# Performance work log

Hardware: AMD Instinct MI355X
Metric: run time of the kernel (lower is better)

## Reference

```python
import jax, jax.numpy as jnp
import numpy as np

B, T, C = 64, 256, 384
H, HD = 6, 64


def setup_inputs() -> dict:
    key = jax.random.key(0)
    ks = jax.random.split(key, 6)
    x = jax.random.normal(ks[0], (B, T, C), dtype=jnp.float32)
    s = 1.0 / np.sqrt(C)
    Wq = jax.random.normal(ks[1], (H, C, HD), dtype=jnp.float32) * s
    Wk = jax.random.normal(ks[2], (H, C, HD), dtype=jnp.float32) * s
    Wv = jax.random.normal(ks[3], (H, C, HD), dtype=jnp.float32) * s
    Wp = jax.random.normal(ks[4], (C, C), dtype=jnp.float32) * s
    bp = jnp.zeros((C,), dtype=jnp.float32)
    return {"x": x, "Wq": Wq, "Wk": Wk, "Wv": Wv, "Wp": Wp, "bp": bp}


def reference(x, Wq, Wk, Wv, Wp, bp):
    # per-head projections (no bias), vectorized over heads
    q = jnp.einsum('btc,hcd->bhtd', x, Wq)
    k = jnp.einsum('btc,hcd->bhtd', x, Wk)
    v = jnp.einsum('btc,hcd->bhtd', x, Wv)
    scale = HD ** (-0.5)
    scores = jnp.einsum('bhtd,bhsd->bhts', q, k) * scale  # [B,H,T,T]
    causal = jnp.tril(jnp.ones((T, T), dtype=bool))
    scores = jnp.where(causal, scores, -jnp.inf)
    wei = jax.nn.softmax(scores, axis=-1)  # dropout is identity in eval mode
    out = jnp.einsum('bhts,bhsd->bhtd', wei, v)
    out = out.transpose(0, 2, 1, 3).reshape(B, T, C)  # concat heads
    return out @ Wp.T + bp
```

## Files before the change

### kernel.cpp

```cpp
#include <hip/hip_runtime.h>
#include <hip/hip_bf16.h>
#include <cstdint>
#include <cstddef>

#define B_ 64
#define T_ 256
#define C_ 384
#define H_ 6
#define HD_ 64

using u16 = unsigned short;
typedef __attribute__((ext_vector_type(8))) short short8;
typedef __attribute__((ext_vector_type(4))) short short4_;
typedef __attribute__((ext_vector_type(4))) float f32x4;

__device__ __forceinline__ u16 f2bf(float f) {
    union { float f; uint32_t u; } x{f};
    uint32_t r = x.u + 0x7fffu + ((x.u >> 16) & 1u);
    return (u16)(r >> 16);
}

__global__ void k_prep(const float* __restrict__ x, const float* __restrict__ Wq,
                       const float* __restrict__ Wk, const float* __restrict__ Wv,
                       const float* __restrict__ Wp, u16* __restrict__ xb,
                       u16* __restrict__ wqkv, u16* __restrict__ wpb) {
    int bid = blockIdx.x;
    if (bid < 3072) {
        int i = (bid * 256 + threadIdx.x) * 8;
        const f32x4* p = (const f32x4*)(x + i);
        f32x4 a = p[0], b = p[1];
        short8 s;
        s[0] = (short)f2bf(a[0]); s[1] = (short)f2bf(a[1]);
        s[2] = (short)f2bf(a[2]); s[3] = (short)f2bf(a[3]);
        s[4] = (short)f2bf(b[0]); s[5] = (short)f2bf(b[1]);
        s[6] = (short)f2bf(b[2]); s[7] = (short)f2bf(b[3]);
        *(short8*)(xb + i) = s;
    } else if (bid < 3180) {
        __shared__ u16 Tt[64 * 65];
        int pb = bid - 3072;
        int which = pb / 36, rem = pb % 36;
        int h = rem / 6, cc0 = (rem % 6) * 64;
        const float* W = (which == 0) ? Wq : ((which == 1) ? Wk : Wv);
        int d = threadIdx.x & 63, cr0 = threadIdx.x >> 6;
#pragma unroll
        for (int p = 0; p < 16; ++p) {
            int cr = p * 4 + cr0;
            Tt[cr * 65 + d] = f2bf(W[(h * 384 + cc0 + cr) * 64 + d]);
        }
        __syncthreads();
        int ccl = threadIdx.x & 63, dl0 = threadIdx.x >> 6;
        int nbase = which * 384 + h * 64;
#pragma unroll
        for (int p = 0; p < 16; ++p) {
            int dl = p * 4 + dl0;
            wqkv[(size_t)(nbase + dl) * 384 + cc0 + ccl] = Tt[ccl * 65 + dl];
        }
    } else {
        int i = ((bid - 3180) * 256 + threadIdx.x) * 8;
        const f32x4* p = (const f32x4*)(Wp + i);
        f32x4 a = p[0], b = p[1];
        short8 s;
        s[0] = (short)f2bf(a[0]); s[1] = (short)f2bf(a[1]);
        s[2] = (short)f2bf(a[2]); s[3] = (short)f2bf(a[3]);
        s[4] = (short)f2bf(b[0]); s[5] = (short)f2bf(b[1]);
        s[6] = (short)f2bf(b[2]); s[7] = (short)f2bf(b[3]);
        *(short8*)(wpb + i) = s;
    }
}

__device__ __forceinline__ void stage_tile(const u16* __restrict__ gbase, int ld,
                                           u16* lds_tile, int wid, int lane, int k0) {
#pragma unroll
    for (int i = 0; i < 4; ++i) {
        int chunk = wid * 4 + i;
        int row = chunk * 8 + (lane >> 3);
        int pslot = lane & 7;
        const u16* gp = gbase + (size_t)row * ld + k0 + ((pslot ^ (row & 7)) << 3);
        u16* lp = lds_tile + chunk * 512;
        __builtin_amdgcn_global_load_lds((const __attribute__((address_space(1))) void*)gp,
                                         (__attribute__((address_space(3))) void*)lp, 16, 0, 0);
    }
}

__device__ __forceinline__ short8 read_frag(const u16* lds_tile, int row, int ks, int g) {
    int pslot = (ks * 4 + g) ^ (row & 7);
    return *(const short8*)&lds_tile[row * 64 + pslot * 8];
}

__global__ __launch_bounds__(256, 2) void k_gemm_qkv(const u16* __restrict__ xb, const u16* __restrict__ wb,
                                                     u16* __restrict__ q, u16* __restrict__ k,
                                                     u16* __restrict__ v) {
    __shared__ alignas(16) u16 lds[2][16384];
    const int tid = threadIdx.x, lane = tid & 63, wid = tid >> 6;
    const int wm = wid >> 1, wn = wid & 1, g = lane >> 4, c = lane & 15;
    const int n0 = blockIdx.x * 128, m0 = blockIdx.y * 128;
    const u16* Ag = xb + (size_t)m0 * 384;
    const u16* Bg = wb + (size_t)n0 * 384;
    f32x4 acc[4][4] = {};
    stage_tile(Ag, 384, &lds[0][0], wid, lane, 0);
    stage_tile(Bg, 384, &lds[0][8192], wid, lane, 0);
    __syncthreads();
    int cur = 0;
    for (int t = 0; t < 6; ++t) {
        if (t < 5) {
            stage_tile(Ag, 384, &lds[cur ^ 1][0], wid, lane, (t + 1) * 64);
            stage_tile(Bg, 384, &lds[cur ^ 1][8192], wid, lane, (t + 1) * 64);
        }
        const u16* A = &lds[cur][0];
        const u16* Bm = &lds[cur][8192];
        short8 af[2][4], bf[2][4];
#pragma unroll
        for (int ks = 0; ks < 2; ++ks) {
#pragma unroll
            for (int mf = 0; mf < 4; ++mf) af[ks][mf] = read_frag(A, wm * 64 + mf * 16 + c, ks, g);
#pragma unroll
            for (int nf = 0; nf < 4; ++nf) bf[ks][nf] = read_frag(Bm, wn * 64 + nf * 16 + c, ks, g);
        }
#pragma unroll
        for (int ks = 0; ks < 2; ++ks)
#pragma unroll
            for (int mf = 0; mf < 4; ++mf)
#pragma unroll
                for (int nf = 0; nf < 4; ++nf)
                    acc[mf][nf] = __builtin_amdgcn_mfma_f32_16x16x32_bf16(af[ks][mf], bf[ks][nf], acc[mf][nf], 0, 0, 0);
        __syncthreads();
        cur ^= 1;
    }
    const int which = n0 / 384;
    u16* dst = (which == 0) ? q : ((which == 1) ? k : v);
    const int h = ((n0 + wn * 64) % 384) / 64;
#pragma unroll
    for (int mf = 0; mf < 4; ++mf)
#pragma unroll
        for (int nf = 0; nf < 4; ++nf)
#pragma unroll
            for (int r = 0; r < 4; ++r) {
                int m = m0 + wm * 64 + mf * 16 + g * 4 + r;
                int d = nf * 16 + c;
                int b = m >> 8, t = m & 255;
                dst[((b * H_ + h) * T_ + t) * HD_ + d] = f2bf(acc[mf][nf][r]);
            }
}

__global__ __launch_bounds__(256, 2) void k_attn(const u16* __restrict__ q, const u16* __restrict__ k,
                                                 const u16* __restrict__ v, u16* __restrict__ ao) {
    __shared__ u16 Kt[64 * 72];
    __shared__ u16 Vt[64 * 72];
    const int tid = threadIdx.x, bh = blockIdx.x;
    const int lane = tid & 63, wid = tid >> 6;
    const int g = lane >> 4, c = lane & 15;
    const int bq = bh * 256;

    short8 qB[4][2];
#pragma unroll
    for (int qf = 0; qf < 4; ++qf)
#pragma unroll
        for (int ks = 0; ks < 2; ++ks) {
            int t = wid * 64 + qf * 16 + c;
            qB[qf][ks] = *(const short8*)&q[(bq + t) * 64 + ks * 32 + g * 8];
        }
    float mrun[4], lrun[4];
#pragma unroll
    for (int i = 0; i < 4; ++i) { mrun[i] = -1e30f; lrun[i] = 0.f; }
    f32x4 o[4][4] = {};

    for (int kt = 0; kt < 4; ++kt) {
#pragma unroll
        for (int i = 0; i < 2; ++i) {
            int idx = tid + i * 256;
            int row = idx >> 3, c8 = (idx & 7) * 8;
            *(short8*)&Kt[row * 72 + c8] = *(const short8*)&k[(bq + kt * 64 + row) * 64 + c8];
            int vrow = idx & 63, vc8 = (idx >> 6) * 8;
            int kv = ((vrow >> 5) << 5) | (((vrow >> 2) & 3) << 3) | (((vrow >> 4) & 1) << 2) | (vrow & 3);
            short8 vv = *(const short8*)&v[(bq + kt * 64 + vrow) * 64 + vc8];
#pragma unroll
            for (int j = 0; j < 8; ++j)
                Vt[(vc8 + j) * 72 + kv] = (u16)vv[j];
        }
        __syncthreads();
        if (kt <= wid) {
            f32x4 st[4][4] = {};
#pragma unroll
            for (int ks = 0; ks < 2; ++ks) {
                short8 kA[4];
#pragma unroll
                for (int sf = 0; sf < 4; ++sf)
                    kA[sf] = *(short8*)&Kt[(sf * 16 + c) * 72 + ks * 32 + g * 8];
#pragma unroll
                for (int sf = 0; sf < 4; ++sf)
#pragma unroll
                    for (int qf = 0; qf < 4; ++qf)
                        st[sf][qf] = __builtin_amdgcn_mfma_f32_16x16x32_bf16(kA[sf], qB[qf][ks], st[sf][qf], 0, 0, 0);
            }
            float pm[4] = {-1e30f, -1e30f, -1e30f, -1e30f};
#pragma unroll
            for (int sf = 0; sf < 4; ++sf)
#pragma unroll
                for (int qf = 0; qf < 4; ++qf)
#pragma unroll
                    for (int r = 0; r < 4; ++r) {
                        float val = st[sf][qf][r] * 0.125f;
                        if (kt == wid) {
                            int s_loc = sf * 16 + g * 4 + r, q_loc = qf * 16 + c;
                            if (s_loc > q_loc) val = -1e30f;
                        }
                        st[sf][qf][r] = val;
                        pm[qf] = fmaxf(pm[qf], val);
                    }
            float alpha[4];
#pragma unroll
            for (int qf = 0; qf < 4; ++qf) {
                pm[qf] = fmaxf(pm[qf], __shfl_xor(pm[qf], 16));
                pm[qf] = fmaxf(pm[qf], __shfl_xor(pm[qf], 32));
                float mnew = fmaxf(mrun[qf], pm[qf]);
                alpha[qf] = __expf(mrun[qf] - mnew);
                mrun[qf] = mnew;
            }
            short8 pA[4][2];
#pragma unroll
            for (int qf = 0; qf < 4; ++qf) {
                float ls = 0.f;
#pragma unroll
                for (int ks = 0; ks < 2; ++ks) {
                    short8 pa;
#pragma unroll
                    for (int half = 0; half < 2; ++half) {
                        f32x4 sv = st[2 * ks + half][qf];
#pragma unroll
                        for (int r = 0; r < 4; ++r) {
                            float p = __expf(sv[r] - mrun[qf]);
                            ls += p;
                            pa[half * 4 + r] = (short)f2bf(p);
                        }
                    }
                    pA[qf][ks] = pa;
                }
                ls += __shfl_xor(ls, 16);
                ls += __shfl_xor(ls, 32);
                lrun[qf] = lrun[qf] * alpha[qf] + ls;
            }
#pragma unroll
            for (int mf = 0; mf < 4; ++mf)
#pragma unroll
                for (int r = 0; r < 4; ++r) {
                    float aof = __shfl(alpha[mf], g * 4 + r);
#pragma unroll
                    for (int df = 0; df < 4; ++df)
                        o[mf][df][r] *= aof;
                }
#pragma unroll
            for (int ks = 0; ks < 2; ++ks) {
                short8 vB[4];
#pragma unroll
                for (int df = 0; df < 4; ++df)
                    vB[df] = *(short8*)&Vt[(df * 16 + c) * 72 + ks * 32 + g * 8];
#pragma unroll
                for (int mf = 0; mf < 4; ++mf)
#pragma unroll
                    for (int df = 0; df < 4; ++df)
                        o[mf][df] = __builtin_amdgcn_mfma_f32_16x16x32_bf16(pA[mf][ks], vB[df], o[mf][df], 0, 0, 0);
            }
        }
        __syncthreads();
    }
    const int bb = bh / H_, hh = bh % H_;
#pragma unroll
    for (int mf = 0; mf < 4; ++mf)
#pragma unroll
        for (int r = 0; r < 4; ++r) {
            float inv = 1.0f / __shfl(lrun[mf], g * 4 + r);
            int t = wid * 64 + mf * 16 + g * 4 + r;
#pragma unroll
            for (int df = 0; df < 4; ++df) {
                int d = df * 16 + c;
                ao[((size_t)(bb * T_ + t)) * C_ + hh * 64 + d] = f2bf(o[mf][df][r] * inv);
            }
        }
}

__global__ __launch_bounds__(256, 2) void k_gemm_proj(const u16* __restrict__ ab, const u16* __restrict__ wp,
                                                      const float* __restrict__ bp, float* __restrict__ out) {
    __shared__ alignas(16) u16 lds[2][16384];
    const int tid = threadIdx.x, lane = tid & 63, wid = tid >> 6;
    const int wm = wid >> 1, wn = wid & 1, g = lane >> 4, c = lane & 15;
    const int n0 = blockIdx.x * 128, m0 = blockIdx.y * 128;
    const u16* Ag = ab + (size_t)m0 * 384;
    const u16* Bg = wp + (size_t)n0 * 384;
    f32x4 acc[4][4] = {};
    stage_tile(Ag, 384, &lds[0][0], wid, lane, 0);
    stage_tile(Bg, 384, &lds[0][8192], wid, lane, 0);
    __syncthreads();
    int cur = 0;
    for (int t = 0; t < 6; ++t) {
        if (t < 5) {
            stage_tile(Ag, 384, &lds[cur ^ 1][0], wid, lane, (t + 1) * 64);
            stage_tile(Bg, 384, &lds[cur ^ 1][8192], wid, lane, (t + 1) * 64);
        }
        const u16* A = &lds[cur][0];
        const u16* Bm = &lds[cur][8192];
        short8 af[2][4], bf[2][4];
#pragma unroll
        for (int ks = 0; ks < 2; ++ks) {
#pragma unroll
            for (int mf = 0; mf < 4; ++mf) af[ks][mf] = read_frag(A, wm * 64 + mf * 16 + c, ks, g);
#pragma unroll
            for (int nf = 0; nf < 4; ++nf) bf[ks][nf] = read_frag(Bm, wn * 64 + nf * 16 + c, ks, g);
        }
#pragma unroll
        for (int ks = 0; ks < 2; ++ks)
#pragma unroll
            for (int mf = 0; mf < 4; ++mf)
#pragma unroll
                for (int nf = 0; nf < 4; ++nf)
                    acc[mf][nf] = __builtin_amdgcn_mfma_f32_16x16x32_bf16(af[ks][mf], bf[ks][nf], acc[mf][nf], 0, 0, 0);
        __syncthreads();
        cur ^= 1;
    }
#pragma unroll
    for (int mf = 0; mf < 4; ++mf)
#pragma unroll
        for (int nf = 0; nf < 4; ++nf)
#pragma unroll
            for (int r = 0; r < 4; ++r) {
                int m = m0 + wm * 64 + mf * 16 + g * 4 + r;
                int n = n0 + wn * 64 + nf * 16 + c;
                out[(size_t)m * C_ + n] = acc[mf][nf][r] + bp[n];
            }
}


extern "C" void kernel_launch(void* const* d_in, const int* in_sizes, int n_in,
                              void* d_out, int out_size, void* d_ws, size_t ws_size,
                              hipStream_t stream) {
    const float* x  = (const float*)d_in[0];
    const float* Wq = (const float*)d_in[1];
    const float* Wk = (const float*)d_in[2];
    const float* Wv = (const float*)d_in[3];
    const float* Wp = (const float*)d_in[4];
    const float* bp = (const float*)d_in[5];
    float* out = (float*)d_out;

    char* ws = (char*)d_ws;
    u16* xb   = (u16*)(ws);
    u16* wqkv = (u16*)(ws + 12582912);
    u16* wpb  = (u16*)(ws + 13467648);
    u16* qb   = (u16*)(ws + 13762560);
    u16* kb   = (u16*)(ws + 26345472);
    u16* vb   = (u16*)(ws + 38928384);
    u16* ab   = (u16*)(ws + 51511296);

    k_prep<<<3252, 256, 0, stream>>>(x, Wq, Wk, Wv, Wp, xb, wqkv, wpb);
    k_gemm_qkv<<<dim3(9, 128), 256, 0, stream>>>(xb, wqkv, qb, kb, vb);
    k_attn<<<384, 256, 0, stream>>>(qb, kb, vb, ab);
    k_gemm_proj<<<dim3(3, 128), 256, 0, stream>>>(ab, wpb, bp, out);
}
```

Before: 74.12 us.

## Fuse QKV projection into the attention kernel, keeping Q/K/V on-chip

Replaces the separate QKV GEMM and attention kernels with a single kernel per (batch, head). Each block computes its head's Q, K and V from the x slice and keeps Q in registers and K/V in LDS. Attention then runs without the Q/K/V global round trip or the extra launch. The cost is that each block re-reads the full x slice for its batch (six heads share it), uses much more LDS at occupancy 1, and has only 384 blocks to spread across the GPU.

```diff
diff --git a/kernel.cpp b/kernel.cpp
--- a/kernel.cpp
+++ b/kernel.cpp
@@ -68,11 +68,12 @@
     }
 }
 
-__device__ __forceinline__ void stage_tile(const u16* __restrict__ gbase, int ld,
+template<int NROWS>
+__device__ __forceinline__ void stage_rows(const u16* __restrict__ gbase, int ld,
                                            u16* lds_tile, int wid, int lane, int k0) {
 #pragma unroll
-    for (int i = 0; i < 4; ++i) {
-        int chunk = wid * 4 + i;
+    for (int i = 0; i < NROWS / 32; ++i) {
+        int chunk = wid * (NROWS / 32) + i;
         int row = chunk * 8 + (lane >> 3);
         int pslot = lane & 7;
         const u16* gp = gbase + (size_t)row * ld + k0 + ((pslot ^ (row & 7)) << 3);
@@ -87,183 +88,193 @@
     return *(const short8*)&lds_tile[row * 64 + pslot * 8];
 }
 
-__global__ __launch_bounds__(256, 2) void k_gemm_qkv(const u16* __restrict__ xb, const u16* __restrict__ wb,
-                                                     u16* __restrict__ q, u16* __restrict__ k,
-                                                     u16* __restrict__ v) {
-    __shared__ alignas(16) u16 lds[2][16384];
+__global__ __launch_bounds__(256, 1) void k_qkv_attn(const u16* __restrict__ xb,
+                                                     const u16* __restrict__ wqkv,
+                                                     u16* __restrict__ ao) {
+    __shared__ alignas(16) u16 Kl[256 * 64];
+    __shared__ alignas(16) u16 Vt[4][64][72];
+    __shared__ alignas(16) u16 xs[256 * 64];
+    __shared__ alignas(16) u16 wsW[2][3][4096];
     const int tid = threadIdx.x, lane = tid & 63, wid = tid >> 6;
-    const int wm = wid >> 1, wn = wid & 1, g = lane >> 4, c = lane & 15;
-    const int n0 = blockIdx.x * 128, m0 = blockIdx.y * 128;
-    const u16* Ag = xb + (size_t)m0 * 384;
-    const u16* Bg = wb + (size_t)n0 * 384;
-    f32x4 acc[4][4] = {};
-    stage_tile(Ag, 384, &lds[0][0], wid, lane, 0);
-    stage_tile(Bg, 384, &lds[0][8192], wid, lane, 0);
+    const int g = lane >> 4, c = lane & 15;
+    const int bh = blockIdx.x, b = bh / H_, h = bh % H_;
+    const u16* xg = xb + (size_t)b * 256 * 384;
+    const u16* wg0 = wqkv + (size_t)(h * 64) * 384;
+    const u16* wg1 = wqkv + (size_t)(384 + h * 64) * 384;
+    const u16* wg2 = wqkv + (size_t)(768 + h * 64) * 384;
+
+    f32x4 aq[4][4] = {}, ak[4][4] = {}, av[4][4] = {};
+
+    stage_rows<256>(xg, 384, xs, wid, lane, 0);
+    stage_rows<64>(wg0, 384, &wsW[0][0][0], wid, lane, 0);
+    stage_rows<64>(wg1, 384, &wsW[0][1][0], wid, lane, 0);
+    stage_rows<64>(wg2, 384, &wsW[0][2][0], wid, lane, 0);
+    asm volatile("s_waitcnt vmcnt(0)" ::: "memory");
+    __builtin_amdgcn_sched_barrier(0);
+    __builtin_amdgcn_s_barrier();
+
+    for (int cc = 0; cc < 6; ++cc) {
+        short8 bx[2][4];
+#pragma unroll
+        for (int ks = 0; ks < 2; ++ks)
+#pragma unroll
+            for (int tf = 0; tf < 4; ++tf)
+                bx[ks][tf] = read_frag(xs, wid * 64 + tf * 16 + c, ks, g);
+        asm volatile("s_waitcnt lgkmcnt(0)" ::: "memory");
+        __builtin_amdgcn_sched_barrier(0);
+        __builtin_amdgcn_s_barrier();
+        if (cc < 5) {
+            stage_rows<256>(xg, 384, xs, wid, lane, (cc + 1) * 64);
+            stage_rows<64>(wg0, 384, &wsW[(cc + 1) & 1][0][0], wid, lane, (cc + 1) * 64);
+            stage_rows<64>(wg1, 384, &wsW[(cc + 1) & 1][1][0], wid, lane, (cc + 1) * 64);
+            stage_rows<64>(wg2, 384, &wsW[(cc + 1) & 1][2][0], wid, lane, (cc + 1) * 64);
+        }
+        const u16* Wql = &wsW[cc & 1][0][0];
+        const u16* Wkl = &wsW[cc & 1][1][0];
+        const u16* Wvl = &wsW[cc & 1][2][0];
+#pragma unroll
+        for (int ks = 0; ks < 2; ++ks) {
+            short8 fq[4], fk[4], fv[4];
+#pragma unroll
+            for (int df = 0; df < 4; ++df) {
+                fq[df] = read_frag(Wql, df * 16 + c, ks, g);
+                fk[df] = read_frag(Wkl, df * 16 + c, ks, g);
+                fv[df] = read_frag(Wvl, df * 16 + c, ks, g);
+            }
+#pragma unroll
+            for (int df = 0; df < 4; ++df)
+#pragma unroll
+                for (int tf = 0; tf < 4; ++tf) {
+                    aq[df][tf] = __builtin_amdgcn_mfma_f32_16x16x32_bf16(fq[df], bx[ks][tf], aq[df][tf], 0, 0, 0);
+                    ak[df][tf] = __builtin_amdgcn_mfma_f32_16x16x32_bf16(fk[df], bx[ks][tf], ak[df][tf], 0, 0, 0);
+                    av[tf][df] = __builtin_amdgcn_mfma_f32_16x16x32_bf16(bx[ks][tf], fv[df], av[tf][df], 0, 0, 0);
+                }
+        }
+        if (cc < 5) asm volatile("s_waitcnt vmcnt(0)" ::: "memory");
+        __builtin_amdgcn_sched_barrier(0);
+        __builtin_amdgcn_s_barrier();
+    }
+
+    short8 qB[4][2];
+#pragma unroll
+    for (int qf = 0; qf < 4; ++qf)
+#pragma unroll
+        for (int ks = 0; ks < 2; ++ks)
+#pragma unroll
+            for (int j = 0; j < 8; ++j)
+                qB[qf][ks][j] = (short)f2bf(aq[2 * ks + (j >> 2)][qf][j & 3]);
+
+#pragma unroll
+    for (int sf = 0; sf < 4; ++sf)
+#pragma unroll
+        for (int df = 0; df < 4; ++df) {
+            int row = wid * 64 + sf * 16 + c;
+            int pslot = (4 * (df >> 1) + g) ^ (row & 7);
+            short4_ k4;
+#pragma unroll
+            for (int r = 0; r < 4; ++r) k4[r] = (short)f2bf(ak[df][sf][r]);
+            *(short4_*)&Kl[row * 64 + pslot * 8 + 4 * (df & 1)] = k4;
+        }
+#pragma unroll
+    for (int sf = 0; sf < 4; ++sf)
+#pragma unroll
+        for (int df = 0; df < 4; ++df) {
+            int colb = 32 * (sf >> 1) + 8 * g + 4 * (sf & 1);
+            short4_ v4;
+#pragma unroll
+            for (int r = 0; r < 4; ++r) v4[r] = (short)f2bf(av[sf][df][r]);
+            *(short4_*)&Vt[wid][df * 16 + c][colb] = v4;
+        }
     __syncthreads();
-    int cur = 0;
-    for (int t = 0; t < 6; ++t) {
-        if (t < 5) {
-            stage_tile(Ag, 384, &lds[cur ^ 1][0], wid, lane, (t + 1) * 64);
-            stage_tile(Bg, 384, &lds[cur ^ 1][8192], wid, lane, (t + 1) * 64);
-        }
-        const u16* A = &lds[cur][0];
-        const u16* Bm = &lds[cur][8192];
-        short8 af[2][4], bf[2][4];
-#pragma unroll
-        for (int ks = 0; ks < 2; ++ks) {
-#pragma unroll
-            for (int mf = 0; mf < 4; ++mf) af[ks][mf] = read_frag(A, wm * 64 + mf * 16 + c, ks, g);
-#pragma unroll
-            for (int nf = 0; nf < 4; ++nf) bf[ks][nf] = read_frag(Bm, wn * 64 + nf * 16 + c, ks, g);
-        }
-#pragma unroll
-        for (int ks = 0; ks < 2; ++ks)
-#pragma unroll
-            for (int mf = 0; mf < 4; ++mf)
-#pragma unroll
-                for (int nf = 0; nf < 4; ++nf)
-                    acc[mf][nf] = __builtin_amdgcn_mfma_f32_16x16x32_bf16(af[ks][mf], bf[ks][nf], acc[mf][nf], 0, 0, 0);
-        __syncthreads();
-        cur ^= 1;
-    }
-    const int which = n0 / 384;
-    u16* dst = (which == 0) ? q : ((which == 1) ? k : v);
-    const int h = ((n0 + wn * 64) % 384) / 64;
-#pragma unroll
-    for (int mf = 0; mf < 4; ++mf)
-#pragma unroll
-        for (int nf = 0; nf < 4; ++nf)
-#pragma unroll
-            for (int r = 0; r < 4; ++r) {
-                int m = m0 + wm * 64 + mf * 16 + g * 4 + r;
-                int d = nf * 16 + c;
-                int b = m >> 8, t = m & 255;
-                dst[((b * H_ + h) * T_ + t) * HD_ + d] = f2bf(acc[mf][nf][r]);
-            }
-}
-
-__global__ __launch_bounds__(256, 2) void k_attn(const u16* __restrict__ q, const u16* __restrict__ k,
-                                                 const u16* __restrict__ v, u16* __restrict__ ao) {
-    __shared__ u16 Kt[64 * 72];
-    __shared__ u16 Vt[64 * 72];
-    const int tid = threadIdx.x, bh = blockIdx.x;
-    const int lane = tid & 63, wid = tid >> 6;
-    const int g = lane >> 4, c = lane & 15;
-    const int bq = bh * 256;
-
-    short8 qB[4][2];
-#pragma unroll
-    for (int qf = 0; qf < 4; ++qf)
-#pragma unroll
-        for (int ks = 0; ks < 2; ++ks) {
-            int t = wid * 64 + qf * 16 + c;
-            qB[qf][ks] = *(const short8*)&q[(bq + t) * 64 + ks * 32 + g * 8];
-        }
+
     float mrun[4], lrun[4];
 #pragma unroll
     for (int i = 0; i < 4; ++i) { mrun[i] = -1e30f; lrun[i] = 0.f; }
     f32x4 o[4][4] = {};
 
-    for (int kt = 0; kt < 4; ++kt) {
-#pragma unroll
-        for (int i = 0; i < 2; ++i) {
-            int idx = tid + i * 256;
-            int row = idx >> 3, c8 = (idx & 7) * 8;
-            *(short8*)&Kt[row * 72 + c8] = *(const short8*)&k[(bq + kt * 64 + row) * 64 + c8];
-            int vrow = idx & 63, vc8 = (idx >> 6) * 8;
-            int kv = ((vrow >> 5) << 5) | (((vrow >> 2) & 3) << 3) | (((vrow >> 4) & 1) << 2) | (vrow & 3);
-            short8 vv = *(const short8*)&v[(bq + kt * 64 + vrow) * 64 + vc8];
-#pragma unroll
-            for (int j = 0; j < 8; ++j)
-                Vt[(vc8 + j) * 72 + kv] = (u16)vv[j];
-        }
-        __syncthreads();
-        if (kt <= wid) {
-            f32x4 st[4][4] = {};
+    for (int kt = 0; kt <= wid; ++kt) {
+        f32x4 st[4][4] = {};
+#pragma unroll
+        for (int ks = 0; ks < 2; ++ks) {
+            short8 kA[4];
+#pragma unroll
+            for (int sf = 0; sf < 4; ++sf)
+                kA[sf] = read_frag(Kl, kt * 64 + sf * 16 + c, ks, g);
+#pragma unroll
+            for (int sf = 0; sf < 4; ++sf)
+#pragma unroll
+                for (int qf = 0; qf < 4; ++qf)
+                    st[sf][qf] = __builtin_amdgcn_mfma_f32_16x16x32_bf16(kA[sf], qB[qf][ks], st[sf][qf], 0, 0, 0);
+        }
+        float pm[4] = {-1e30f, -1e30f, -1e30f, -1e30f};
+#pragma unroll
+        for (int sf = 0; sf < 4; ++sf)
+#pragma unroll
+            for (int qf = 0; qf < 4; ++qf)
+#pragma unroll
+                for (int r = 0; r < 4; ++r) {
+                    float val = st[sf][qf][r] * 0.125f;
+                    if (kt == wid) {
+                        int s_loc = sf * 16 + g * 4 + r, q_loc = qf * 16 + c;
+                        if (s_loc > q_loc) val = -1e30f;
+                    }
+                    st[sf][qf][r] = val;
+                    pm[qf] = fmaxf(pm[qf], val);
+                }
+        float alpha[4];
+#pragma unroll
+        for (int qf = 0; qf < 4; ++qf) {
+            pm[qf] = fmaxf(pm[qf], __shfl_xor(pm[qf], 16));
+            pm[qf] = fmaxf(pm[qf], __shfl_xor(pm[qf], 32));
+            float mnew = fmaxf(mrun[qf], pm[qf]);
+            alpha[qf] = __expf(mrun[qf] - mnew);
+            mrun[qf] = mnew;
+        }
+        short8 pA[4][2];
+#pragma unroll
+        for (int qf = 0; qf < 4; ++qf) {
+            float ls = 0.f;
 #pragma unroll
             for (int ks = 0; ks < 2; ++ks) {
-                short8 kA[4];
-#pragma unroll
-                for (int sf = 0; sf < 4; ++sf)
-                    kA[sf] = *(short8*)&Kt[(sf * 16 + c) * 72 + ks * 32 + g * 8];
-#pragma unroll
-                for (int sf = 0; sf < 4; ++sf)
-#pragma unroll
-                    for (int qf = 0; qf < 4; ++qf)
-                        st[sf][qf] = __builtin_amdgcn_mfma_f32_16x16x32_bf16(kA[sf], qB[qf][ks], st[sf][qf], 0, 0, 0);
-            }
-            float pm[4] = {-1e30f, -1e30f, -1e30f, -1e30f};
-#pragma unroll
-            for (int sf = 0; sf < 4; ++sf)
-#pragma unroll
-                for (int qf = 0; qf < 4; ++qf)
+                short8 pa;
+#pragma unroll
+                for (int half = 0; half < 2; ++half) {
+                    f32x4 sv = st[2 * ks + half][qf];
 #pragma unroll
                     for (int r = 0; r < 4; ++r) {
-                        float val = st[sf][qf][r] * 0.125f;
-                        if (kt == wid) {
-                            int s_loc = sf * 16 + g * 4 + r, q_loc = qf * 16 + c;
-                            if (s_loc > q_loc) val = -1e30f;
-                        }
-                        st[sf][qf][r] = val;
-                        pm[qf] = fmaxf(pm[qf], val);
+                        float p = __expf(sv[r] - mrun[qf]);
+                        ls += p;
+                        pa[half * 4 + r] = (short)f2bf(p);
                     }
-            float alpha[4];
-#pragma unroll
-            for (int qf = 0; qf < 4; ++qf) {
-                pm[qf] = fmaxf(pm[qf], __shfl_xor(pm[qf], 16));
-                pm[qf] = fmaxf(pm[qf], __shfl_xor(pm[qf], 32));
-                float mnew = fmaxf(mrun[qf], pm[qf]);
-                alpha[qf] = __expf(mrun[qf] - mnew);
-                mrun[qf] = mnew;
-            }
-            short8 pA[4][2];
-#pragma unroll
-            for (int qf = 0; qf < 4; ++qf) {
-                float ls = 0.f;
-#pragma unroll
-                for (int ks = 0; ks < 2; ++ks) {
-                    short8 pa;
-#pragma unroll
-                    for (int half = 0; half < 2; ++half) {
-                        f32x4 sv = st[2 * ks + half][qf];
-#pragma unroll
-                        for (int r = 0; r < 4; ++r) {
-                            float p = __expf(sv[r] - mrun[qf]);
-                            ls += p;
-                            pa[half * 4 + r] = (short)f2bf(p);
-                        }
-                    }
-                    pA[qf][ks] = pa;
                 }
-                ls += __shfl_xor(ls, 16);
-                ls += __shfl_xor(ls, 32);
-                lrun[qf] = lrun[qf] * alpha[qf] + ls;
-            }
+                pA[qf][ks] = pa;
+            }
+            ls += __shfl_xor(ls, 16);
+            ls += __shfl_xor(ls, 32);
+            lrun[qf] = lrun[qf] * alpha[qf] + ls;
+        }
+#pragma unroll
+        for (int mf = 0; mf < 4; ++mf)
+#pragma unroll
+            for (int r = 0; r < 4; ++r) {
+                float aof = __shfl(alpha[mf], g * 4 + r);
+#pragma unroll
+                for (int df = 0; df < 4; ++df)
+                    o[mf][df][r] *= aof;
+            }
+#pragma unroll
+        for (int ks = 0; ks < 2; ++ks) {
+            short8 vB[4];
+#pragma unroll
+            for (int df = 0; df < 4; ++df)
+                vB[df] = *(short8*)&Vt[kt][df * 16 + c][ks * 32 + g * 8];
 #pragma unroll
             for (int mf = 0; mf < 4; ++mf)
 #pragma unroll
-                for (int r = 0; r < 4; ++r) {
-                    float aof = __shfl(alpha[mf], g * 4 + r);
-#pragma unroll
-                    for (int df = 0; df < 4; ++df)
-                        o[mf][df][r] *= aof;
-                }
-#pragma unroll
-            for (int ks = 0; ks < 2; ++ks) {
-                short8 vB[4];
-#pragma unroll
                 for (int df = 0; df < 4; ++df)
-                    vB[df] = *(short8*)&Vt[(df * 16 + c) * 72 + ks * 32 + g * 8];
-#pragma unroll
-                for (int mf = 0; mf < 4; ++mf)
-#pragma unroll
-                    for (int df = 0; df < 4; ++df)
-                        o[mf][df] = __builtin_amdgcn_mfma_f32_16x16x32_bf16(pA[mf][ks], vB[df], o[mf][df], 0, 0, 0);
-            }
-        }
-        __syncthreads();
-    }
-    const int bb = bh / H_, hh = bh % H_;
+                    o[mf][df] = __builtin_amdgcn_mfma_f32_16x16x32_bf16(pA[mf][ks], vB[df], o[mf][df], 0, 0, 0);
+        }
+    }
 #pragma unroll
     for (int mf = 0; mf < 4; ++mf)
 #pragma unroll
@@ -273,9 +284,14 @@
 #pragma unroll
             for (int df = 0; df < 4; ++df) {
                 int d = df * 16 + c;
-                ao[((size_t)(bb * T_ + t)) * C_ + hh * 64 + d] = f2bf(o[mf][df][r] * inv);
-            }
-        }
+                ao[((size_t)(b * T_ + t)) * C_ + h * 64 + d] = f2bf(o[mf][df][r] * inv);
+            }
+        }
+}
+
+__device__ __forceinline__ void stage_tile(const u16* __restrict__ gbase, int ld,
+                                           u16* lds_tile, int wid, int lane, int k0) {
+    stage_rows<128>(gbase, ld, lds_tile, wid, lane, k0);
 }
 
 __global__ __launch_bounds__(256, 2) void k_gemm_proj(const u16* __restrict__ ab, const u16* __restrict__ wp,
@@ -344,13 +360,9 @@
     u16* xb   = (u16*)(ws);
     u16* wqkv = (u16*)(ws + 12582912);
     u16* wpb  = (u16*)(ws + 13467648);
-    u16* qb   = (u16*)(ws + 13762560);
-    u16* kb   = (u16*)(ws + 26345472);
-    u16* vb   = (u16*)(ws + 38928384);
-    u16* ab   = (u16*)(ws + 51511296);
+    u16* ab   = (u16*)(ws + 13762560);
 
     k_prep<<<3252, 256, 0, stream>>>(x, Wq, Wk, Wv, Wp, xb, wqkv, wpb);
-    k_gemm_qkv<<<dim3(9, 128), 256, 0, stream>>>(xb, wqkv, qb, kb, vb);
-    k_attn<<<384, 256, 0, stream>>>(qb, kb, vb, ab);
+    k_qkv_attn<<<384, 256, 0, stream>>>(xb, wqkv, ab);
     k_gemm_proj<<<dim3(3, 128), 256, 0, stream>>>(ab, wpb, bp, out);
 }
```

After: 80.79 us. +9.0%, slower.
